# Kernel optimization log

Measured on AMD Instinct MI355X. Metric: run time of the kernel, lower is better.

## Reference

```python
import jax, jax.numpy as jnp
import numpy as np

N_NODES = 15279  # hardcoded in the original forward's reshape


def spmm(rows, cols, vals, dense):
    # sparse [N,N] @ dense [N,F] via gather + segment-sum over COO edges
    gathered = dense[cols] * vals[:, None]          # [E, F]
    return jax.ops.segment_sum(gathered, rows, num_segments=N_NODES)


def setup_inputs() -> dict:
    key = jax.random.key(0)
    ks = jax.random.split(key, 10)
    E = 488928  # 15279 nodes * avg_degree 32
    emb_num, emb_dim = 10000, 128
    in_ch, n_hid, n_class = 1024, 512, 16

    x = jax.random.randint(ks[0], (N_NODES, 8), 0, emb_num, dtype=jnp.int64)
    adj_rows = jax.random.randint(ks[1], (E,), 0, N_NODES, dtype=jnp.int32)
    adj_cols = jax.random.randint(ks[2], (E,), 0, N_NODES, dtype=jnp.int32)
    adj_vals = jax.random.uniform(ks[3], (E,), dtype=jnp.float32)

    emb_table = jax.random.normal(ks[4], (emb_num + 1, emb_dim), dtype=jnp.float32) * 0.02
    emb_table = emb_table.at[0].set(0.0)  # padding_idx=0

    # Kipf GraphConvolution init: uniform(-1/sqrt(fan_out), 1/sqrt(fan_out))
    s1 = 1.0 / np.sqrt(n_hid)
    W1 = jax.random.uniform(ks[5], (in_ch, n_hid), minval=-s1, maxval=s1, dtype=jnp.float32)
    b1 = jax.random.uniform(ks[6], (n_hid,), minval=-s1, maxval=s1, dtype=jnp.float32)
    s2 = 1.0 / np.sqrt(n_class)
    W2 = jax.random.uniform(ks[7], (n_hid, n_class), minval=-s2, maxval=s2, dtype=jnp.float32)
    b2 = jax.random.uniform(ks[8], (n_class,), minval=-s2, maxval=s2, dtype=jnp.float32)

    return {"x": x, "adj_rows": adj_rows, "adj_cols": adj_cols, "adj_vals": adj_vals,
            "emb_table": emb_table, "W1": W1, "b1": b1, "W2": W2, "b2": b2}


def reference(x, adj_rows, adj_cols, adj_vals, emb_table, W1, b1, W2, b2):
    # embedding lookup + relu, flatten to [15279, in_ch]
    h = jax.nn.relu(emb_table[x])                  # [N, 8, emb_dim]
    h = h.reshape(N_NODES, -1)                     # [N, in_ch]
    # gc1: adj @ (h @ W1) + b1, then relu (dropout is identity in eval)
    h = jax.nn.relu(spmm(adj_rows, adj_cols, adj_vals, h @ W1) + b1)
    # gc2: adj @ (h @ W2) + b2
    return spmm(adj_rows, adj_cols, adj_vals, h @ W2) + b2
```

## Files before the change

kernel.cpp:

```cpp
#include <hip/hip_runtime.h>

#define NNODES 15279
#define NEDGE  488928
#define INCH   1024
#define NHID   512
#define NCLS   16
#define EMBROWS 10001
#define BCAP   128

#define NB_EMBR 1251
#define NB_W1T  128
#define NB_GEMM1 960
#define NB_SCAT 1910

using short8 = __attribute__((ext_vector_type(8))) short;
using f32x4  = __attribute__((ext_vector_type(4))) float;
using f32x2  = __attribute__((ext_vector_type(2))) float;

__device__ __forceinline__ float asf(unsigned int u) {
  union { unsigned int i; float f; } v; v.i = u; return v.f;
}
__device__ __forceinline__ unsigned short f2bf(float f) {
  union { float ff; unsigned int i; } v; v.ff = f;
  return (unsigned short)((v.i + 0x7FFFu + ((v.i >> 16) & 1u)) >> 16);
}

__global__ __launch_bounds__(256) void k_prep(const float* __restrict__ emb,
                                              unsigned short* __restrict__ embr,
                                              const float* __restrict__ W1,
                                              unsigned short* __restrict__ w1t) {
  __shared__ float tile[64][65];
  int b = blockIdx.x;
  int t = threadIdx.x;
  if (b < NB_EMBR) {
    int g = b * 256 + t;
    if (g * 4 < EMBROWS * 128) {
      const float4 v = *(const float4*)&emb[g * 4];
      unsigned int lo = (unsigned int)f2bf(fmaxf(v.x, 0.f)) | ((unsigned int)f2bf(fmaxf(v.y, 0.f)) << 16);
      unsigned int hi = (unsigned int)f2bf(fmaxf(v.z, 0.f)) | ((unsigned int)f2bf(fmaxf(v.w, 0.f)) << 16);
      uint2 o; o.x = lo; o.y = hi;
      *(uint2*)&embr[g * 4] = o;
    }
  } else {
    int b2 = b - NB_EMBR;
    int k0 = (b2 & 15) * 64, n0 = (b2 >> 4) * 64;
    int c = t & 63, r4 = t >> 6;
    for (int i = 0; i < 16; ++i) {
      int r = r4 + i * 4;
      tile[r][c] = W1[(k0 + r) * NHID + n0 + c];
    }
    __syncthreads();
    for (int i = 0; i < 16; ++i) {
      int nr = r4 + i * 4;
      w1t[(size_t)(n0 + nr) * INCH + k0 + c] = f2bf(tile[c][nr]);
    }
  }
}

__global__ __launch_bounds__(256) void k_gemm1_scatter(
    const int* __restrict__ x,
    const unsigned short* __restrict__ embr,
    const unsigned short* __restrict__ Bt,
    unsigned short* __restrict__ Cs,
    const int* __restrict__ rows,
    const int* __restrict__ cols,
    const float* __restrict__ vals,
    int* __restrict__ cursor,
    unsigned int* __restrict__ bpack) {
  __shared__ unsigned short As[128 * 64];
  __shared__ unsigned short Bs[64 * 64];
  const int t = threadIdx.x;
  if (blockIdx.x >= NB_GEMM1) {
    int e = (blockIdx.x - NB_GEMM1) * 256 + t;
    if (e < NEDGE) {
      int r = rows[e];
      int idx = atomicAdd(&cursor[r], 1);
      if (idx < BCAP) {
        bpack[r * BCAP + idx] = ((unsigned int)cols[e] << 16) | (unsigned int)f2bf(vals[e]);
      }
    }
    return;
  }
  const int m0 = (blockIdx.x >> 3) * 128;
  const int n0 = (blockIdx.x & 7) * 64;
  const int w = t >> 6, l = t & 63;
  const int wm = w >> 1, wn = w & 1;
  const int l4 = l >> 4, l15 = l & 15;
  const int rowA = wm * 64 + l15;
  const int colB = wn * 32 + l15;
  f32x4 acc[4][2] = {};

  int xidx[4][8];
#pragma unroll
  for (int i = 0; i < 4; ++i) {
    int grow = m0 + (t >> 3) + i * 32;
    grow = grow < NNODES ? grow : NNODES - 1;
    *(int4*)&xidx[i][0] = *(const int4*)&x[grow * 8];
    *(int4*)&xidx[i][4] = *(const int4*)&x[grow * 8 + 4];
  }

#pragma unroll
  for (int kt = 0; kt < 16; ++kt) {
    const int k0 = kt * 64;
    const int s = kt >> 1;
    const int dbase = (kt & 1) * 64;
#pragma unroll
    for (int i = 0; i < 4; ++i) {
      int p = i * 256 + t;
      int row = i * 32 + (t >> 3);
      int skg = ((t & 7) ^ (row & 7)) * 8;
      __builtin_amdgcn_global_load_lds(
          (const __attribute__((address_space(1))) void*)&embr[(size_t)xidx[i][s] * 128 + dbase + skg],
          (__attribute__((address_space(3))) void*)&As[p * 8], 16, 0, 0);
    }
#pragma unroll
    for (int i = 0; i < 2; ++i) {
      int p = i * 256 + t;
      int row = i * 32 + (t >> 3);
      int skg = ((t & 7) ^ (row & 7)) * 8;
      __builtin_amdgcn_global_load_lds(
          (const __attribute__((address_space(1))) void*)&Bt[(size_t)(n0 + row) * INCH + k0 + skg],
          (__attribute__((address_space(3))) void*)&Bs[p * 8], 16, 0, 0);
    }
    __syncthreads();
#pragma unroll
    for (int kk = 0; kk < 2; ++kk) {
      short8 af[4], bfr[2];
#pragma unroll
      for (int m = 0; m < 4; ++m) {
        int r = rowA + m * 16;
        af[m] = *(const short8*)&As[(r * 8 + ((kk * 4 + l4) ^ (r & 7))) * 8];
      }
#pragma unroll
      for (int n = 0; n < 2; ++n) {
        int c = colB + n * 16;
        bfr[n] = *(const short8*)&Bs[(c * 8 + ((kk * 4 + l4) ^ (c & 7))) * 8];
      }
#pragma unroll
      for (int m = 0; m < 4; ++m)
#pragma unroll
        for (int n = 0; n < 2; ++n)
          acc[m][n] = __builtin_amdgcn_mfma_f32_16x16x32_bf16(af[m], bfr[n], acc[m][n], 0, 0, 0);
    }
    __syncthreads();
  }
  const int rb = m0 + wm * 64 + l4 * 4;
  const int cb = wn * 32 + l15;
  unsigned short* Cb = Cs + (size_t)(n0 >> 6) * NNODES * 64;
#pragma unroll
  for (int m = 0; m < 4; ++m)
#pragma unroll
    for (int j = 0; j < 4; ++j) {
      int r = rb + m * 16 + j;
      if (r < NNODES) {
        Cb[(size_t)r * 64 + cb]      = f2bf(acc[m][0][j]);
        Cb[(size_t)r * 64 + cb + 16] = f2bf(acc[m][1][j]);
      }
    }
}

__global__ __launch_bounds__(256) void k_spmm1(const int* __restrict__ cnt,
                                               const unsigned int* __restrict__ bpack,
                                               const unsigned short* __restrict__ t1s,
                                               const float* __restrict__ b1,
                                               unsigned short* __restrict__ h1) {
  int b = blockIdx.x;
  int slice = b & 7;
  int rgrp = b >> 3;
  int t = threadIdx.x;
  int wid = t >> 6, lane = t & 63;
  int rloc = lane >> 4, el = (lane >> 3) & 1, ft = lane & 7;
  int r = rgrp * 16 + wid * 4 + rloc;
  bool valid = r < NNODES;
  int rr = valid ? r : NNODES - 1;
  const char* tbase = (const char*)(t1s + (size_t)slice * NNODES * 64) + ft * 16;
  int fglob = slice * 64 + ft * 8;
  int e0 = rr * BCAP;
  int c0n = cnt[rr]; c0n = c0n < BCAP ? c0n : BCAP;
  int e1 = valid ? e0 + c0n : e0;
  f32x2 acc[4] = {};
  int p = e0 + el;

#define GFMA4(U0, U1, U2, U3) do {                                          \
    uint4 g0 = *(const uint4*)(tbase + ((size_t)((U0) >> 16) << 7));        \
    uint4 g1 = *(const uint4*)(tbase + ((size_t)((U1) >> 16) << 7));        \
    uint4 g2 = *(const uint4*)(tbase + ((size_t)((U2) >> 16) << 7));        \
    uint4 g3 = *(const uint4*)(tbase + ((size_t)((U3) >> 16) << 7));        \
    float v0 = asf((U0) << 16), v1 = asf((U1) << 16);                       \
    float v2 = asf((U2) << 16), v3 = asf((U3) << 16);                       \
    f32x2 w0 = {v0, v0}, w1 = {v1, v1}, w2 = {v2, v2}, w3 = {v3, v3};       \
    unsigned int a0[4] = {g0.x, g0.y, g0.z, g0.w};                          \
    unsigned int a1[4] = {g1.x, g1.y, g1.z, g1.w};                          \
    unsigned int a2[4] = {g2.x, g2.y, g2.z, g2.w};                          \
    unsigned int a3[4] = {g3.x, g3.y, g3.z, g3.w};                          \
    _Pragma("unroll")                                                       \
    for (int d = 0; d < 4; ++d) {                                           \
      f32x2 p0 = {asf(a0[d] << 16), asf(a0[d] & 0xffff0000u)};              \
      f32x2 p1 = {asf(a1[d] << 16), asf(a1[d] & 0xffff0000u)};              \
      f32x2 p2 = {asf(a2[d] << 16), asf(a2[d] & 0xffff0000u)};              \
      f32x2 p3 = {asf(a3[d] << 16), asf(a3[d] & 0xffff0000u)};              \
      acc[d] += w0 * p0;                                                    \
      acc[d] += w1 * p1;                                                    \
      acc[d] += w2 * p2;                                                    \
      acc[d] += w3 * p3;                                                    \
    }                                                                       \
  } while (0)

  if (p + 6 < e1) {
    unsigned int u0 = bpack[p], u1 = bpack[p + 2], u2 = bpack[p + 4], u3 = bpack[p + 6];
    int q = p + 8;
    for (; q + 6 < e1; q += 8) {
      unsigned int n0 = bpack[q],     n1 = bpack[q + 2];
      unsigned int n2 = bpack[q + 4], n3 = bpack[q + 6];
      GFMA4(u0, u1, u2, u3);
      u0 = n0; u1 = n1; u2 = n2; u3 = n3;
    }
    GFMA4(u0, u1, u2, u3);
    p = q;
  }
  for (; p < e1; p += 2) {
    unsigned int u = bpack[p];
    uint4 a = *(const uint4*)(tbase + ((size_t)(u >> 16) << 7));
    float v = asf(u << 16);
    f32x2 v2 = {v, v};
    unsigned int ua[4] = {a.x, a.y, a.z, a.w};
#pragma unroll
    for (int d = 0; d < 4; ++d) {
      f32x2 pp = {asf(ua[d] << 16), asf(ua[d] & 0xffff0000u)};
      acc[d] += v2 * pp;
    }
  }
#undef GFMA4
#pragma unroll
  for (int d = 0; d < 4; ++d) {
    acc[d].x += __shfl_xor(acc[d].x, 8);
    acc[d].y += __shfl_xor(acc[d].y, 8);
  }
  if (el == 0 && valid) {
    unsigned int o[4];
#pragma unroll
    for (int d = 0; d < 4; ++d) {
      float s0 = fmaxf(acc[d].x + b1[fglob + 2 * d], 0.f);
      float s1 = fmaxf(acc[d].y + b1[fglob + 2 * d + 1], 0.f);
      o[d] = (unsigned int)f2bf(s0) | ((unsigned int)f2bf(s1) << 16);
    }
    uint4 ov; ov.x = o[0]; ov.y = o[1]; ov.z = o[2]; ov.w = o[3];
    *(uint4*)&h1[(size_t)r * NHID + fglob] = ov;
  }
}

__global__ __launch_bounds__(256) void k_gemm2(const unsigned short* __restrict__ h1,
                                               const float* __restrict__ W2,
                                               float* __restrict__ t2) {
  __shared__ unsigned short w2t[16 * 520];
  int t = threadIdx.x;
#pragma unroll
  for (int i = 0; i < 32; ++i) {
    int p = i * 256 + t;
    int k = p >> 4, f = p & 15;
    w2t[f * 520 + k] = f2bf(W2[p]);
  }
  int w = t >> 6, l = t & 63;
  int l15 = l & 15, l4 = l >> 4;
  int r0 = blockIdx.x * 64 + w * 16;
  int row = r0 + l15; row = row < NNODES ? row : NNODES - 1;
  short8 af[16];
#pragma unroll
  for (int kk = 0; kk < 16; ++kk)
    af[kk] = *(const short8*)&h1[(size_t)row * NHID + kk * 32 + l4 * 8];
  __syncthreads();
  f32x4 acc = {};
#pragma unroll
  for (int kk = 0; kk < 16; ++kk) {
    short8 bfr = *(const short8*)&w2t[l15 * 520 + kk * 32 + l4 * 8];
    acc = __builtin_amdgcn_mfma_f32_16x16x32_bf16(af[kk], bfr, acc, 0, 0, 0);
  }
#pragma unroll
  for (int j = 0; j < 4; ++j) {
    int r = r0 + l4 * 4 + j;
    if (r < NNODES) t2[(size_t)r * NCLS + l15] = acc[j];
  }
}

__global__ __launch_bounds__(256) void k_spmm2(const int* __restrict__ cnt,
                                               const unsigned int* __restrict__ bpack,
                                               const float* __restrict__ t2,
                                               const float* __restrict__ b2,
                                               float* __restrict__ out) {
  int t = threadIdx.x;
  int f = t & 15, rl = t >> 4;
  int r = blockIdx.x * 16 + rl;
  if (r >= NNODES) return;
  const char* t2b = (const char*)t2 + f * 4;
  int e0 = r * BCAP;
  int n = cnt[r]; n = n < BCAP ? n : BCAP;
  int e1 = e0 + n;
  float a0 = 0.f, a1 = 0.f, a2 = 0.f, a3 = 0.f;
  int e = e0;
  for (; e + 3 < e1; e += 4) {
    unsigned int u0 = bpack[e], u1 = bpack[e + 1], u2 = bpack[e + 2], u3 = bpack[e + 3];
    a0 += asf(u0 << 16) * *(const float*)(t2b + ((size_t)(u0 >> 16) << 6));
    a1 += asf(u1 << 16) * *(const float*)(t2b + ((size_t)(u1 >> 16) << 6));
    a2 += asf(u2 << 16) * *(const float*)(t2b + ((size_t)(u2 >> 16) << 6));
    a3 += asf(u3 << 16) * *(const float*)(t2b + ((size_t)(u3 >> 16) << 6));
  }
  for (; e < e1; ++e) {
    unsigned int u = bpack[e];
    a0 += asf(u << 16) * *(const float*)(t2b + ((size_t)(u >> 16) << 6));
  }
  out[(size_t)r * NCLS + f] = (a0 + a1) + (a2 + a3) + b2[f];
}

extern "C" void kernel_launch(void* const* d_in, const int* in_sizes, int n_in,
                              void* d_out, int out_size, void* d_ws, size_t ws_size,
                              hipStream_t stream) {
  (void)in_sizes; (void)n_in; (void)out_size; (void)ws_size;
  const int*   x    = (const int*)  d_in[0];
  const int*   rows = (const int*)  d_in[1];
  const int*   cols = (const int*)  d_in[2];
  const float* vals = (const float*)d_in[3];
  const float* emb  = (const float*)d_in[4];
  const float* W1   = (const float*)d_in[5];
  const float* b1   = (const float*)d_in[6];
  const float* W2   = (const float*)d_in[7];
  const float* b2   = (const float*)d_in[8];
  float* out = (float*)d_out;

  char* ws = (char*)d_ws;
  size_t off = 0;
  auto take = [&](size_t bytes) {
    char* p = ws + off;
    off = (off + bytes + 255) & ~(size_t)255;
    return p;
  };
  unsigned short* embr = (unsigned short*)take((size_t)EMBROWS * 128 * 2);
  unsigned short* w1t  = (unsigned short*)take((size_t)NHID * INCH * 2);
  unsigned short* t1s  = (unsigned short*)take((size_t)NNODES * NHID * 2);
  unsigned short* h1   = (unsigned short*)take((size_t)NNODES * NHID * 2);
  float*          t2   = (float*)take((size_t)NNODES * NCLS * 4);
  int*            cursor = (int*)take((size_t)NNODES * 4);
  unsigned int*   bpack  = (unsigned int*)take((size_t)NNODES * BCAP * 4);

  hipMemsetAsync(cursor, 0, (size_t)NNODES * 4, stream);

  k_prep<<<NB_EMBR + NB_W1T, 256, 0, stream>>>(emb, embr, W1, w1t);
  k_gemm1_scatter<<<NB_GEMM1 + NB_SCAT, 256, 0, stream>>>(
      x, embr, w1t, t1s, rows, cols, vals, cursor, bpack);
  k_spmm1<<<((NNODES + 15) / 16) * 8, 256, 0, stream>>>(cursor, bpack, t1s, b1, h1);
  k_gemm2<<<(NNODES + 63) / 64, 256, 0, stream>>>(h1, W2, t2);
  k_spmm2<<<(NNODES + 15) / 16, 256, 0, stream>>>(cursor, bpack, t2, b2, out);
}
```

Baseline: 97.02 us.

## Fold cursor memset into prep kernel and widen gemm1 K-tile to 128

```diff
diff --git a/kernel.cpp b/kernel.cpp
--- a/kernel.cpp
+++ b/kernel.cpp
@@ -10,6 +10,7 @@
 
 #define NB_EMBR 1251
 #define NB_W1T  128
+#define NB_CURS 60
 #define NB_GEMM1 960
 #define NB_SCAT 1910
 
@@ -28,7 +29,8 @@
 __global__ __launch_bounds__(256) void k_prep(const float* __restrict__ emb,
                                               unsigned short* __restrict__ embr,
                                               const float* __restrict__ W1,
-                                              unsigned short* __restrict__ w1t) {
+                                              unsigned short* __restrict__ w1t,
+                                              int* __restrict__ cursor) {
   __shared__ float tile[64][65];
   int b = blockIdx.x;
   int t = threadIdx.x;
@@ -41,7 +43,7 @@
       uint2 o; o.x = lo; o.y = hi;
       *(uint2*)&embr[g * 4] = o;
     }
-  } else {
+  } else if (b < NB_EMBR + NB_W1T) {
     int b2 = b - NB_EMBR;
     int k0 = (b2 & 15) * 64, n0 = (b2 >> 4) * 64;
     int c = t & 63, r4 = t >> 6;
@@ -54,6 +56,9 @@
       int nr = r4 + i * 4;
       w1t[(size_t)(n0 + nr) * INCH + k0 + c] = f2bf(tile[c][nr]);
     }
+  } else {
+    int n = (b - NB_EMBR - NB_W1T) * 256 + t;
+    if (n < NNODES) cursor[n] = 0;
   }
 }
 
@@ -67,8 +72,8 @@
     const float* __restrict__ vals,
     int* __restrict__ cursor,
     unsigned int* __restrict__ bpack) {
-  __shared__ unsigned short As[128 * 64];
-  __shared__ unsigned short Bs[64 * 64];
+  __shared__ unsigned short As[128 * 128];
+  __shared__ unsigned short Bs[64 * 128];
   const int t = threadIdx.x;
   if (blockIdx.x >= NB_GEMM1) {
     int e = (blockIdx.x - NB_GEMM1) * 256 + t;
@@ -90,51 +95,41 @@
   const int colB = wn * 32 + l15;
   f32x4 acc[4][2] = {};
 
-  int xidx[4][8];
-#pragma unroll
-  for (int i = 0; i < 4; ++i) {
-    int grow = m0 + (t >> 3) + i * 32;
-    grow = grow < NNODES ? grow : NNODES - 1;
-    *(int4*)&xidx[i][0] = *(const int4*)&x[grow * 8];
-    *(int4*)&xidx[i][4] = *(const int4*)&x[grow * 8 + 4];
-  }
-
-#pragma unroll
-  for (int kt = 0; kt < 16; ++kt) {
-    const int k0 = kt * 64;
-    const int s = kt >> 1;
-    const int dbase = (kt & 1) * 64;
+#pragma unroll
+  for (int kt = 0; kt < 8; ++kt) {
+#pragma unroll
+    for (int i = 0; i < 8; ++i) {
+      int idx = i * 256 + t;
+      int row = idx >> 4, kg = idx & 15;
+      int skg = (kg ^ (row & 7)) * 8;
+      int ga = m0 + row; ga = ga < NNODES ? ga : NNODES - 1;
+      int xi = x[ga * 8 + kt];
+      __builtin_amdgcn_global_load_lds(
+          (const __attribute__((address_space(1))) void*)&embr[(size_t)xi * 128 + skg],
+          (__attribute__((address_space(3))) void*)&As[idx * 8], 16, 0, 0);
+    }
 #pragma unroll
     for (int i = 0; i < 4; ++i) {
-      int p = i * 256 + t;
-      int row = i * 32 + (t >> 3);
-      int skg = ((t & 7) ^ (row & 7)) * 8;
+      int idx = i * 256 + t;
+      int row = idx >> 4, kg = idx & 15;
+      int skg = (kg ^ (row & 7)) * 8;
       __builtin_amdgcn_global_load_lds(
-          (const __attribute__((address_space(1))) void*)&embr[(size_t)xidx[i][s] * 128 + dbase + skg],
-          (__attribute__((address_space(3))) void*)&As[p * 8], 16, 0, 0);
-    }
-#pragma unroll
-    for (int i = 0; i < 2; ++i) {
-      int p = i * 256 + t;
-      int row = i * 32 + (t >> 3);
-      int skg = ((t & 7) ^ (row & 7)) * 8;
-      __builtin_amdgcn_global_load_lds(
-          (const __attribute__((address_space(1))) void*)&Bt[(size_t)(n0 + row) * INCH + k0 + skg],
-          (__attribute__((address_space(3))) void*)&Bs[p * 8], 16, 0, 0);
+          (const __attribute__((address_space(1))) void*)&Bt[(size_t)(n0 + row) * INCH + kt * 128 + skg],
+          (__attribute__((address_space(3))) void*)&Bs[idx * 8], 16, 0, 0);
     }
     __syncthreads();
 #pragma unroll
-    for (int kk = 0; kk < 2; ++kk) {
+    for (int kk = 0; kk < 4; ++kk) {
       short8 af[4], bfr[2];
 #pragma unroll
       for (int m = 0; m < 4; ++m) {
         int r = rowA + m * 16;
-        af[m] = *(const short8*)&As[(r * 8 + ((kk * 4 + l4) ^ (r & 7))) * 8];
+        af[m] = *(const short8*)&As[(r * 16 + ((kk * 4 + l4) ^ (r & 7))) * 8];
       }
 #pragma unroll
       for (int n = 0; n < 2; ++n) {
         int c = colB + n * 16;
-        bfr[n] = *(const short8*)&Bs[(c * 8 + ((kk * 4 + l4) ^ (c & 7))) * 8];
+        bfr[n] = *(const short8*)&Bs[(c * 16 + ((kk * 4 + l4) ^ (c & 7))) * 8];
       }
 #pragma unroll
       for (int m = 0; m < 4; ++m)
@@ -341,9 +336,7 @@
   int*            cursor = (int*)take((size_t)NNODES * 4);
   unsigned int*   bpack  = (unsigned int*)take((size_t)NNODES * BCAP * 4);
 
-  hipMemsetAsync(cursor, 0, (size_t)NNODES * 4, stream);
-
-  k_prep<<<NB_EMBR + NB_W1T, 256, 0, stream>>>(emb, embr, W1, w1t);
+  k_prep<<<NB_EMBR + NB_W1T + NB_CURS, 256, 0, stream>>>(emb, embr, W1, w1t, cursor);
   k_gemm1_scatter<<<NB_GEMM1 + NB_SCAT, 256, 0, stream>>>(
       x, embr, w1t, t1s, rows, cols, vals, cursor, bpack);
   k_spmm1<<<((NNODES + 15) / 16) * 8, 256, 0, stream>>>(cursor, bpack, t1s, b1, h1);
```

After: 94.33 us. 2.8% less time.

## Register-prefetch next K tile in gemm1 and fold cursor memset into prep

Applied to the files above, without the earlier changes.

```diff
diff --git a/kernel.cpp b/kernel.cpp
--- a/kernel.cpp
+++ b/kernel.cpp
@@ -10,6 +10,7 @@
 
 #define NB_EMBR 1251
 #define NB_W1T  128
+#define NB_CURS 60
 #define NB_GEMM1 960
 #define NB_SCAT 1910
 
@@ -28,7 +29,8 @@
 __global__ __launch_bounds__(256) void k_prep(const float* __restrict__ emb,
                                               unsigned short* __restrict__ embr,
                                               const float* __restrict__ W1,
-                                              unsigned short* __restrict__ w1t) {
+                                              unsigned short* __restrict__ w1t,
+                                              int* __restrict__ cursor) {
   __shared__ float tile[64][65];
   int b = blockIdx.x;
   int t = threadIdx.x;
@@ -41,7 +43,7 @@
       uint2 o; o.x = lo; o.y = hi;
       *(uint2*)&embr[g * 4] = o;
     }
-  } else {
+  } else if (b < NB_EMBR + NB_W1T) {
     int b2 = b - NB_EMBR;
     int k0 = (b2 & 15) * 64, n0 = (b2 >> 4) * 64;
     int c = t & 63, r4 = t >> 6;
@@ -54,6 +56,9 @@
       int nr = r4 + i * 4;
       w1t[(size_t)(n0 + nr) * INCH + k0 + c] = f2bf(tile[c][nr]);
     }
+  } else {
+    int n = (b - NB_EMBR - NB_W1T) * 256 + t;
+    if (n < NNODES) cursor[n] = 0;
   }
 }
 
@@ -98,31 +103,39 @@
     *(int4*)&xidx[i][0] = *(const int4*)&x[grow * 8];
     *(int4*)&xidx[i][4] = *(const int4*)&x[grow * 8 + 4];
   }
-
+  const int skg = ((t & 7) ^ ((t >> 3) & 7)) * 8;
+  const int pA0 = t * 8;
+  const size_t bOff = (size_t)(n0 + (t >> 3)) * INCH + skg;
+
+  uint4 ra[4], rb[2];
+
+#define REGLOAD(KT) do {                                                             \
+    const int s_ = (KT) >> 1;                                                        \
+    const int db_ = ((KT) & 1) * 64;                                                 \
+    const int k0_ = (KT) * 64;                                                       \
+    _Pragma("unroll")                                                                \
+    for (int i_ = 0; i_ < 4; ++i_)                                                   \
+      ra[i_] = *(const uint4*)&embr[(size_t)xidx[i_][s_] * 128 + db_ + skg];         \
+    _Pragma("unroll")                                                                \
+    for (int i_ = 0; i_ < 2; ++i_)                                                   \
+      rb[i_] = *(const uint4*)&Bt[bOff + (size_t)i_ * 32 * INCH + k0_];              \
+  } while (0)
+
+#define LDSWRITE() do {                                                              \
+    _Pragma("unroll")                                                                \
+    for (int i_ = 0; i_ < 4; ++i_)                                                   \
+      *(uint4*)&As[(i_ * 256) * 8 + pA0] = ra[i_];                                   \
+    _Pragma("unroll")                                                                \
+    for (int i_ = 0; i_ < 2; ++i_)                                                   \
+      *(uint4*)&Bs[(i_ * 256) * 8 + pA0] = rb[i_];                                   \
+  } while (0)
+
+  REGLOAD(0);
+  LDSWRITE();
+  __syncthreads();
 #pragma unroll
   for (int kt = 0; kt < 16; ++kt) {
-    const int k0 = kt * 64;
-    const int s = kt >> 1;
-    const int dbase = (kt & 1) * 64;
-#pragma unroll
-    for (int i = 0; i < 4; ++i) {
-      int p = i * 256 + t;
-      int row = i * 32 + (t >> 3);
-      int skg = ((t & 7) ^ (row & 7)) * 8;
-      __builtin_amdgcn_global_load_lds(
-          (const __attribute__((address_space(1))) void*)&embr[(size_t)xidx[i][s] * 128 + dbase + skg],
-          (__attribute__((address_space(3))) void*)&As[p * 8], 16, 0, 0);
-    }
-#pragma unroll
-    for (int i = 0; i < 2; ++i) {
-      int p = i * 256 + t;
-      int row = i * 32 + (t >> 3);
-      int skg = ((t & 7) ^ (row & 7)) * 8;
-      __builtin_amdgcn_global_load_lds(
-          (const __attribute__((address_space(1))) void*)&Bt[(size_t)(n0 + row) * INCH + k0 + skg],
-          (__attribute__((address_space(3))) void*)&Bs[p * 8], 16, 0, 0);
-    }
-    __syncthreads();
+    if (kt + 1 < 16) REGLOAD(kt + 1);
 #pragma unroll
     for (int kk = 0; kk < 2; ++kk) {
       short8 af[4], bfr[2];
@@ -143,15 +156,21 @@
           acc[m][n] = __builtin_amdgcn_mfma_f32_16x16x32_bf16(af[m], bfr[n], acc[m][n], 0, 0, 0);
     }
     __syncthreads();
-  }
-  const int rb = m0 + wm * 64 + l4 * 4;
+    if (kt + 1 < 16) {
+      LDSWRITE();
+      __syncthreads();
+    }
+  }
+#undef REGLOAD
+#undef LDSWRITE
+  const int rb2 = m0 + wm * 64 + l4 * 4;
   const int cb = wn * 32 + l15;
   unsigned short* Cb = Cs + (size_t)(n0 >> 6) * NNODES * 64;
 #pragma unroll
   for (int m = 0; m < 4; ++m)
 #pragma unroll
     for (int j = 0; j < 4; ++j) {
-      int r = rb + m * 16 + j;
+      int r = rb2 + m * 16 + j;
       if (r < NNODES) {
         Cb[(size_t)r * 64 + cb]      = f2bf(acc[m][0][j]);
         Cb[(size_t)r * 64 + cb + 16] = f2bf(acc[m][1][j]);
@@ -341,9 +360,7 @@
   int*            cursor = (int*)take((size_t)NNODES * 4);
   unsigned int*   bpack  = (unsigned int*)take((size_t)NNODES * BCAP * 4);
 
-  hipMemsetAsync(cursor, 0, (size_t)NNODES * 4, stream);
-
-  k_prep<<<NB_EMBR + NB_W1T, 256, 0, stream>>>(emb, embr, W1, w1t);
+  k_prep<<<NB_EMBR + NB_W1T + NB_CURS, 256, 0, stream>>>(emb, embr, W1, w1t, cursor);
   k_gemm1_scatter<<<NB_GEMM1 + NB_SCAT, 256, 0, stream>>>(
       x, embr, w1t, t1s, rows, cols, vals, cursor, bpack);
   k_spmm1<<<((NNODES + 15) / 16) * 8, 256, 0, stream>>>(cursor, bpack, t1s, b1, h1);
```

Result: slower. 165.1 us (+70.2%).
